# Performance work log

Measured on AMD Instinct MI355X. Metric: run time of the kernel, lower is better.

The kernel has to match this reference:

```python
import jax, jax.numpy as jnp
import numpy as np

N, F, H, C, E = 20000, 512, 128, 64, 640000


def _uniform(key, shape, stdv):
    return jax.random.uniform(key, shape, jnp.float32, -stdv, stdv)


def setup_inputs() -> dict:
    key = jax.random.key(0)
    ks = jax.random.split(key, 20)
    inp = {}
    for i, name in enumerate(['x1', 'x2', 'x3']):
        inp[name] = jax.random.normal(ks[i], (N, F), jnp.float32)
    for v, base in zip([1, 2, 3], [3, 6, 9]):
        inp[f'src{v}'] = jax.random.randint(ks[base], (E,), 0, N, jnp.int32)
        inp[f'dst{v}'] = jax.random.randint(ks[base + 1], (E,), 0, N, jnp.int32)
        inp[f'val{v}'] = jax.random.uniform(ks[base + 2], (E,), jnp.float32)
    s1 = 1.0 / np.sqrt(H)
    s2 = 1.0 / np.sqrt(C)
    sv = 1.0 / np.sqrt(3.0)
    inp['W1'] = _uniform(ks[12], (3, 3, F, H), s1)   # [gc, view_role, F, H]
    inp['wv1'] = _uniform(ks[13], (3, 3), sv)
    inp['b1'] = _uniform(ks[14], (3, H), sv)
    inp['W2'] = _uniform(ks[15], (3, 3, H, C), s2)
    inp['wv2'] = _uniform(ks[16], (3, 3), sv)
    inp['b2'] = _uniform(ks[17], (3, C), sv)
    return inp


def _spmm(src, dst, val, emb, n):
    # out[i] = sum_{edges e with src=i} val[e] * emb[dst[e]]
    return jax.ops.segment_sum(val[:, None] * emb[dst], src, num_segments=n)


def _igc(xs, adjs, W, wv, b, n):
    # xs: [x_self, x_v2, x_v3]; adjs: matching [(src,dst,val)]*3
    embs = [xs[i] @ W[i] for i in range(3)]
    neigh = [_spmm(adjs[i][0], adjs[i][1], adjs[i][2], embs[i], n) for i in range(3)]
    agg = wv[0] * neigh[0] + wv[1] * neigh[1] + wv[2] * neigh[2]
    return embs[0] + 1.01 * agg + b


def reference(x1, x2, x3, src1, dst1, val1, src2, dst2, val2, src3, dst3, val3,
              W1, wv1, b1, W2, wv2, b2):
    n = x1.shape[0]
    a1, a2, a3 = (src1, dst1, val1), (src2, dst2, val2), (src3, dst3, val3)
    relu = jax.nn.relu
    h1 = relu(_igc([x1, x2, x3], [a1, a2, a3], W1[0], wv1[0], b1[0], n))
    h2 = relu(_igc([x2, x1, x3], [a2, a1, a3], W1[1], wv1[1], b1[1], n))
    h3 = relu(_igc([x3, x1, x2], [a3, a1, a2], W1[2], wv1[2], b1[2], n))
    y1 = relu(_igc([h1, h2, h3], [a1, a2, a3], W2[0], wv2[0], b2[0], n))
    y2 = relu(_igc([h2, h1, h3], [a2, a1, a3], W2[1], wv2[1], b2[1], n))
    y3 = relu(_igc([h3, h1, h2], [a3, a1, a2], W2[2], wv2[2], b2[2], n))
    return jnp.abs((y1 + y2 + y3) / 3.0)
```

## Files before the change

### kernel.cpp

```cpp
#include <hip/hip_runtime.h>
#include <hip/hip_bf16.h>

#define N_NODES 20000
#define F_DIM   512
#define H_DIM   128
#define C_DIM   64
#define E_EDGES 640000

#define P_WV1   64
#define P_B1    80
#define P_WV2   464
#define P_B2    480
#define P_E     1024
#define P_H     (P_E + 3*N_NODES*H_DIM)
#define P_YSUM  (P_H + 3*N_NODES*H_DIM)
#define RP_SZ      20032
#define CSR_STRIDE (RP_SZ + 2*E_EDGES)
#define P_CSR   (P_YSUM + N_NODES*C_DIM)
#define P_CUR   (P_CSR + 3*CSR_STRIDE)
#define P_WT1   (P_E + 4000000)
#define P_WT2   (P_E + 4300000)
#define P_W1H   (P_YSUM)
#define P_W1L   (P_YSUM + 294912)
#define P_W2H   (P_E + 4000000)
#define P_W2L   (P_E + 4050000)
#define DEG_STRIDE 20480

typedef __attribute__((ext_vector_type(8))) unsigned short u16x8;
typedef __attribute__((ext_vector_type(8))) __bf16 bf16x8;
typedef __attribute__((ext_vector_type(4))) float f32x4;

__device__ inline float cvt(float x) { return x; }
__device__ inline float cvt(__hip_bfloat16 x) { return __bfloat162float(x); }

__device__ inline void store_out(float v, float* p) { *p = v; }
__device__ inline void store_out(float v, __hip_bfloat16* p) { *p = __float2bfloat16(v); }

__device__ inline unsigned short f2bf_bits(float x) {
    __hip_bfloat16 b = __float2bfloat16(x);
    return *(unsigned short*)&b;
}
__device__ inline void splitbf(float x, unsigned short& h, unsigned short& l) {
    h = f2bf_bits(x);
    float hf = __uint_as_float(((unsigned int)h) << 16);
    l = f2bf_bits(x - hf);
}

__global__ void detect_kernel(const unsigned short* __restrict__ x, int* flag) {
    __shared__ int cnt;
    if (threadIdx.x == 0) cnt = 0;
    __syncthreads();
    int c = 0;
    for (int i = threadIdx.x; i < 4096; i += 256) {
        int ex = (x[i] >> 7) & 0xff;
        if (ex >= 140) c++;
    }
    atomicAdd(&cnt, c);
    __syncthreads();
    if (threadIdx.x == 0) *flag = (cnt > 64) ? 1 : 0;
}

__global__ void prep_kernel(const int* __restrict__ flag,
                            const void* wv1, const void* b1,
                            const void* wv2, const void* b2, float* ws) {
    bool f32 = (*flag == 1);
    int t = threadIdx.x;
    auto get = [&](const void* p, int i) -> float {
        return f32 ? ((const float*)p)[i]
                   : __bfloat162float(((const __hip_bfloat16*)p)[i]);
    };
    if (t < 9) ws[P_WV1 + t] = get(wv1, t);
    if (t < 9) ws[P_WV2 + t] = get(wv2, t);
    for (int i = t; i < 3*H_DIM; i += 256) ws[P_B1 + i] = get(b1, i);
    for (int i = t; i < 3*C_DIM; i += 256) ws[P_B2 + i] = get(b2, i);
}

__global__ __launch_bounds__(256)
void hist3_kernel(const int* __restrict__ s0, const int* __restrict__ s1,
                  const int* __restrict__ s2, int* __restrict__ deg) {
    int e = blockIdx.x * 256 + threadIdx.x;
    if (e >= E_EDGES) return;
    const int* s = (blockIdx.y == 0) ? s0 : (blockIdx.y == 1) ? s1 : s2;
    atomicAdd(&deg[blockIdx.y * DEG_STRIDE + s[e]], 1);
}

__global__ __launch_bounds__(256)
void scan3_kernel(const int* __restrict__ degBase, int* __restrict__ rpBase) {
    __shared__ int sums[256];
    const int* deg = degBase + blockIdx.x * DEG_STRIDE;
    int* rowptr = rpBase + (long)blockIdx.x * CSR_STRIDE;
    const int CHUNK = 79;
    int t = threadIdx.x;
    int beg = t * CHUNK;
    int end = beg + CHUNK; if (end > N_NODES) end = N_NODES;
    int s = 0;
    for (int i = beg; i < end && i < N_NODES; ++i) s += deg[i];
    sums[t] = s;
    __syncthreads();
    for (int off = 1; off < 256; off <<= 1) {
        int v = (t >= off) ? sums[t - off] : 0;
        __syncthreads();
        sums[t] += v;
        __syncthreads();
    }
    int run = sums[t] - s;
    for (int i = beg; i < end && i < N_NODES; ++i) {
        rowptr[i] = run;
        run += deg[i];
    }
    if (t == 255) rowptr[N_NODES] = run;
}

__global__ __launch_bounds__(256)
void fill3_kernel(const int* __restrict__ flag,
                  const int* __restrict__ s0, const int* __restrict__ d0,
                  const void* __restrict__ v0,
                  const int* __restrict__ s1, const int* __restrict__ d1,
                  const void* __restrict__ v1,
                  const int* __restrict__ s2, const int* __restrict__ d2,
                  const void* __restrict__ v2,
                  int* __restrict__ rpBase, int* __restrict__ curBase) {
    int e = blockIdx.x * 256 + threadIdx.x;
    if (e >= E_EDGES) return;
    const int z = blockIdx.y;
    const int* src = (z == 0) ? s0 : (z == 1) ? s1 : s2;
    const int* dst = (z == 0) ? d0 : (z == 1) ? d1 : d2;
    const void* val = (z == 0) ? v0 : (z == 1) ? v1 : v2;
    float v = (*flag == 1) ? ((const float*)val)[e]
                           : __bfloat162float(((const __hip_bfloat16*)val)[e]);
    int s = src[e];
    int* rowptr = rpBase + (long)z * CSR_STRIDE;
    int pos = rowptr[s] + atomicAdd(&curBase[z * DEG_STRIDE + s], 1);
    int2* ed = (int2*)(rpBase + (long)z * CSR_STRIDE + RP_SZ);
    ed[pos] = make_int2(dst[e], __float_as_int(v));
}

__global__ __launch_bounds__(256)
void transpose_w_kernel(const int* __restrict__ flag,
                        const void* __restrict__ Wsrc,
                        unsigned short* __restrict__ Wt, int K, int HO) {
    if (*flag != 0) return;
    __shared__ unsigned short T[64][80];
    const unsigned short* W = (const unsigned short*)Wsrc + (long)blockIdx.z * K * HO;
    unsigned short* O = Wt + (long)blockIdx.z * HO * K;
    const int k0 = blockIdx.x * 64, n0 = blockIdx.y * 64;
    const int t = threadIdx.x;
    const int rr = t >> 3, cc = (t & 7) * 8;
    #pragma unroll
    for (int i = 0; i < 2; ++i) {
        int k = rr + i * 32;
        *(u16x8*)&T[k][cc] = *(const u16x8*)&W[(long)(k0 + k) * HO + n0 + cc];
    }
    __syncthreads();
    #pragma unroll
    for (int i = 0; i < 2; ++i) {
        int nn = rr + i * 32;
        u16x8 v;
        #pragma unroll
        for (int j = 0; j < 8; ++j) v[j] = T[cc + j][nn];
        *(u16x8*)&O[(long)(n0 + nn) * K + k0 + cc] = v;
    }
}

__global__ __launch_bounds__(256)
void split_w_kernel(const int* __restrict__ flag,
                    const float* __restrict__ Wsrc,
                    unsigned short* __restrict__ Wh,
                    unsigned short* __restrict__ Wl, int K, int HO) {
    if (*flag != 1) return;
    __shared__ float T[64][68];
    const float* W = Wsrc + (long)blockIdx.z * K * HO;
    unsigned short* Oh = Wh + (long)blockIdx.z * HO * K;
    unsigned short* Ol = Wl + (long)blockIdx.z * HO * K;
    const int k0 = blockIdx.x * 64, n0 = blockIdx.y * 64;
    const int t = threadIdx.x;
    #pragma unroll
    for (int i = 0; i < 16; ++i) {
        int idx = t + i * 256;
        int r = idx >> 6, c = idx & 63;
        T[r][c] = W[(long)(k0 + r) * HO + n0 + c];
    }
    __syncthreads();
    #pragma unroll
    for (int i = 0; i < 16; ++i) {
        int idx = t + i * 256;
        int nn = idx >> 6, kk = idx & 63;
        unsigned short h, l;
        splitbf(T[kk][nn], h, l);
        Oh[(long)(n0 + nn) * K + k0 + kk] = h;
        Ol[(long)(n0 + nn) * K + k0 + kk] = l;
    }
}

#define SWZ(r, kb) (((r) << 7) + ((kb) ^ (((r) & 7) << 4)))

__global__ __launch_bounds__(256)
void gemm_mfma1_kernel(const int* __restrict__ flag,
                       const unsigned short* __restrict__ x0,
                       const unsigned short* __restrict__ x1,
                       const unsigned short* __restrict__ x2,
                       const unsigned short* __restrict__ WtBase,
                       unsigned short* __restrict__ outBase, int n) {
    if (*flag != 0) return;
    const int role = blockIdx.y;
    const unsigned short* X = (role == 0) ? x0 : (role == 1) ? x1 : x2;
    const unsigned short* Wt = WtBase + (long)role * H_DIM * F_DIM;
    unsigned short* out = outBase + (long)role * N_NODES * H_DIM;
    __shared__ __align__(16) unsigned short As[64 * 64];
    __shared__ __align__(16) unsigned short Bs[128 * 64];
    const int t = threadIdx.x;
    const int lane = t & 63;
    const int wave = t >> 6;
    const int wm = wave & 1, wn = wave >> 1;
    const int row0 = blockIdx.x * 64;
    const int rl = lane & 15;
    const int kq = lane >> 4;
    const int sr = t >> 3;
    const int sc = (t & 7) * 8;
    f32x4 acc[2][4] = {};
    for (int k0 = 0; k0 < F_DIM; k0 += 64) {
        #pragma unroll
        for (int i = 0; i < 2; ++i) {
            int r = i * 32 + sr;
            int gr = row0 + r; if (gr >= n) gr = n - 1;
            u16x8 v = *(const u16x8*)&X[(long)gr * F_DIM + k0 + sc];
            *(u16x8*)((char*)As + SWZ(r, sc * 2)) = v;
        }
        #pragma unroll
        for (int i = 0; i < 4; ++i) {
            int r = i * 32 + sr;
            u16x8 v = *(const u16x8*)&Wt[(long)r * F_DIM + k0 + sc];
            *(u16x8*)((char*)Bs + SWZ(r, sc * 2)) = v;
        }
        __syncthreads();
        #pragma unroll
        for (int s = 0; s < 2; ++s) {
            const int kb = s * 64 + kq * 16;
            bf16x8 af[2], bfr[4];
            #pragma unroll
            for (int mi = 0; mi < 2; ++mi) {
                int r = wm * 32 + mi * 16 + rl;
                af[mi] = *(const bf16x8*)((const char*)As + SWZ(r, kb));
            }
            #pragma unroll
            for (int ni = 0; ni < 4; ++ni) {
                int r = wn * 64 + ni * 16 + rl;
                bfr[ni] = *(const bf16x8*)((const char*)Bs + SWZ(r, kb));
            }
            #pragma unroll
            for (int mi = 0; mi < 2; ++mi)
                #pragma unroll
                for (int ni = 0; ni < 4; ++ni)
                    acc[mi][ni] = __builtin_amdgcn_mfma_f32_16x16x32_bf16(
                        af[mi], bfr[ni], acc[mi][ni], 0, 0, 0);
        }
        __syncthreads();
    }
    #pragma unroll
    for (int mi = 0; mi < 2; ++mi) {
        #pragma unroll
        for (int q = 0; q < 4; ++q) {
            int row = row0 + wm * 32 + mi * 16 + kq * 4 + q;
            if (row < n) {
                #pragma unroll
                for (int ni = 0; ni < 4; ++ni) {
                    int col = wn * 64 + ni * 16 + rl;
                    out[(long)row * H_DIM + col] = f2bf_bits(acc[mi][ni][q]);
                }
            }
        }
    }
}

__global__ __launch_bounds__(256)
void gemm_mfma1f_kernel(const int* __restrict__ flag,
                        const float* __restrict__ x0,
                        const float* __restrict__ x1,
                        const float* __restrict__ x2,
                        const unsigned short* __restrict__ WhBase,
                        const unsigned short* __restrict__ WlBase,
                        float* __restrict__ outBase, int n) {
    if (*flag != 1) return;
    const int role = blockIdx.y;
    const float* X = (role == 0) ? x0 : (role == 1) ? x1 : x2;
    const unsigned short* Wh = WhBase + (long)role * H_DIM * F_DIM;
    const unsigned short* Wl = WlBase + (long)role * H_DIM * F_DIM;
    float* out = outBase + (long)role * N_NODES * H_DIM;
    __shared__ __align__(16) unsigned short Ash[64 * 64];
    __shared__ __align__(16) unsigned short Asl[64 * 64];
    __shared__ __align__(16) unsigned short Bsh[128 * 64];
    __shared__ __align__(16) unsigned short Bsl[128 * 64];
    const int t = threadIdx.x;
    const int lane = t & 63;
    const int wave = t >> 6;
    const int wm = wave & 1, wn = wave >> 1;
    const int row0 = blockIdx.x * 64;
    const int rl = lane & 15;
    const int kq = lane >> 4;
    const int sr = t >> 3;
    const int sc = (t & 7) * 8;
    f32x4 acc[2][4] = {};
    for (int k0 = 0; k0 < F_DIM; k0 += 64) {
        #pragma unroll
        for (int i = 0; i < 2; ++i) {
            int r = i * 32 + sr;
            int gr = row0 + r; if (gr >= n) gr = n - 1;
            float4 v0 = *(const float4*)&X[(long)gr * F_DIM + k0 + sc];
            float4 v1 = *(const float4*)&X[(long)gr * F_DIM + k0 + sc + 4];
            float xs[8] = {v0.x, v0.y, v0.z, v0.w, v1.x, v1.y, v1.z, v1.w};
            u16x8 hi, lo;
            #pragma unroll
            for (int j = 0; j < 8; ++j) { unsigned short h, l; splitbf(xs[j], h, l); hi[j] = h; lo[j] = l; }
            *(u16x8*)((char*)Ash + SWZ(r, sc * 2)) = hi;
            *(u16x8*)((char*)Asl + SWZ(r, sc * 2)) = lo;
        }
        #pragma unroll
        for (int i = 0; i < 4; ++i) {
            int r = i * 32 + sr;
            u16x8 vh = *(const u16x8*)&Wh[(long)r * F_DIM + k0 + sc];
            u16x8 vl = *(const u16x8*)&Wl[(long)r * F_DIM + k0 + sc];
            *(u16x8*)((char*)Bsh + SWZ(r, sc * 2)) = vh;
            *(u16x8*)((char*)Bsl + SWZ(r, sc * 2)) = vl;
        }
        __syncthreads();
        #pragma unroll
        for (int s = 0; s < 2; ++s) {
            const int kb = s * 64 + kq * 16;
            bf16x8 ah[2], al[2], bh[4], bl[4];
            #pragma unroll
            for (int mi = 0; mi < 2; ++mi) {
                int r = wm * 32 + mi * 16 + rl;
                ah[mi] = *(const bf16x8*)((const char*)Ash + SWZ(r, kb));
                al[mi] = *(const bf16x8*)((const char*)Asl + SWZ(r, kb));
            }
            #pragma unroll
            for (int ni = 0; ni < 4; ++ni) {
                int r = wn * 64 + ni * 16 + rl;
                bh[ni] = *(const bf16x8*)((const char*)Bsh + SWZ(r, kb));
                bl[ni] = *(const bf16x8*)((const char*)Bsl + SWZ(r, kb));
            }
            #pragma unroll
            for (int mi = 0; mi < 2; ++mi)
                #pragma unroll
                for (int ni = 0; ni < 4; ++ni) {
                    acc[mi][ni] = __builtin_amdgcn_mfma_f32_16x16x32_bf16(
                        ah[mi], bh[ni], acc[mi][ni], 0, 0, 0);
                    acc[mi][ni] = __builtin_amdgcn_mfma_f32_16x16x32_bf16(
                        ah[mi], bl[ni], acc[mi][ni], 0, 0, 0);
                    acc[mi][ni] = __builtin_amdgcn_mfma_f32_16x16x32_bf16(
                        al[mi], bh[ni], acc[mi][ni], 0, 0, 0);
                }
        }
        __syncthreads();
    }
    #pragma unroll
    for (int mi = 0; mi < 2; ++mi) {
        #pragma unroll
        for (int q = 0; q < 4; ++q) {
            int row = row0 + wm * 32 + mi * 16 + kq * 4 + q;
            if (row < n) {
                #pragma unroll
                for (int ni = 0; ni < 4; ++ni) {
                    int col = wn * 64 + ni * 16 + rl;
                    out[(long)row * H_DIM + col] = acc[mi][ni][q];
                }
            }
        }
    }
}

#define SWZ2(r, kb) (((r) << 8) + ((kb) ^ (((r) & 7) << 4)))

__global__ __launch_bounds__(256)
void gemm_mfma2_kernel(const int* __restrict__ flag,
                       const unsigned short* __restrict__ h0,
                       const unsigned short* __restrict__ h1,
                       const unsigned short* __restrict__ h2,
                       const unsigned short* __restrict__ WtBase,
                       unsigned short* __restrict__ outBase, int n) {
    if (*flag != 0) return;
    const int role = blockIdx.y;
    const unsigned short* X = (role == 0) ? h0 : (role == 1) ? h1 : h2;
    const unsigned short* Wt = WtBase + (long)role * C_DIM * H_DIM;
    unsigned short* out = outBase + (long)role * N_NODES * C_DIM;
    __shared__ __align__(16) unsigned short As[64 * 128];
    __shared__ __align__(16) unsigned short Bs[64 * 128];
    const int t = threadIdx.x;
    const int lane = t & 63;
    const int wave = t >> 6;
    const int wm = wave & 1, wn = wave >> 1;
    const int row0 = blockIdx.x * 64;
    const int rl = lane & 15;
    const int kq = lane >> 4;
    #pragma unroll
    for (int i = 0; i < 4; ++i) {
        int e = t + i * 256;
        int r = e >> 4, c8 = e & 15;
        int gr = row0 + r; if (gr >= n) gr = n - 1;
        u16x8 va = *(const u16x8*)&X[(long)gr * H_DIM + c8 * 8];
        *(u16x8*)((char*)As + SWZ2(r, c8 * 16)) = va;
        u16x8 vb = *(const u16x8*)&Wt[(long)r * H_DIM + c8 * 8];
        *(u16x8*)((char*)Bs + SWZ2(r, c8 * 16)) = vb;
    }
    __syncthreads();
    f32x4 acc[2][2] = {};
    #pragma unroll
    for (int s = 0; s < 4; ++s) {
        const int kb = s * 64 + kq * 16;
        bf16x8 af[2], bfr[2];
        #pragma unroll
        for (int mi = 0; mi < 2; ++mi) {
            int r = wm * 32 + mi * 16 + rl;
            af[mi] = *(const bf16x8*)((const char*)As + SWZ2(r, kb));
        }
        #pragma unroll
        for (int ni = 0; ni < 2; ++ni) {
            int r = wn * 32 + ni * 16 + rl;
            bfr[ni] = *(const bf16x8*)((const char*)Bs + SWZ2(r, kb));
        }
        #pragma unroll
        for (int mi = 0; mi < 2; ++mi)
            #pragma unroll
            for (int ni = 0; ni < 2; ++ni)
                acc[mi][ni] = __builtin_amdgcn_mfma_f32_16x16x32_bf16(
                    af[mi], bfr[ni], acc[mi][ni], 0, 0, 0);
    }
    #pragma unroll
    for (int mi = 0; mi < 2; ++mi) {
        #pragma unroll
        for (int q = 0; q < 4; ++q) {
            int row = row0 + wm * 32 + mi * 16 + kq * 4 + q;
            if (row < n) {
                #pragma unroll
                for (int ni = 0; ni < 2; ++ni) {
                    int col = wn * 32 + ni * 16 + rl;
                    out[(long)row * C_DIM + col] = f2bf_bits(acc[mi][ni][q]);
                }
            }
        }
    }
}

__global__ __launch_bounds__(256)
void gemm_mfma2f_kernel(const int* __restrict__ flag,
                        const float* __restrict__ h0,
                        const float* __restrict__ h1,
                        const float* __restrict__ h2,
                        const unsigned short* __restrict__ WhBase,
                        const unsigned short* __restrict__ WlBase,
                        float* __restrict__ outBase, int n) {
    if (*flag != 1) return;
    const int role = blockIdx.y;
    const float* X = (role == 0) ? h0 : (role == 1) ? h1 : h2;
    const unsigned short* Wh = WhBase + (long)role * C_DIM * H_DIM;
    const unsigned short* Wl = WlBase + (long)role * C_DIM * H_DIM;
    float* out = outBase + (long)role * N_NODES * C_DIM;
    __shared__ __align__(16) unsigned short Ash[64 * 128];
    __shared__ __align__(16) unsigned short Asl[64 * 128];
    __shared__ __align__(16) unsigned short Bsh[64 * 128];
    __shared__ __align__(16) unsigned short Bsl[64 * 128];
    const int t = threadIdx.x;
    const int lane = t & 63;
    const int wave = t >> 6;
    const int wm = wave & 1, wn = wave >> 1;
    const int row0 = blockIdx.x * 64;
    const int rl = lane & 15;
    const int kq = lane >> 4;
    #pragma unroll
    for (int i = 0; i < 4; ++i) {
        int e = t + i * 256;
        int r = e >> 4, c8 = e & 15;
        int gr = row0 + r; if (gr >= n) gr = n - 1;
        float4 v0 = *(const float4*)&X[(long)gr * H_DIM + c8 * 8];
        float4 v1 = *(const float4*)&X[(long)gr * H_DIM + c8 * 8 + 4];
        float xs[8] = {v0.x, v0.y, v0.z, v0.w, v1.x, v1.y, v1.z, v1.w};
        u16x8 hi, lo;
        #pragma unroll
        for (int j = 0; j < 8; ++j) { unsigned short h, l; splitbf(xs[j], h, l); hi[j] = h; lo[j] = l; }
        *(u16x8*)((char*)Ash + SWZ2(r, c8 * 16)) = hi;
        *(u16x8*)((char*)Asl + SWZ2(r, c8 * 16)) = lo;
        u16x8 vh = *(const u16x8*)&Wh[(long)r * H_DIM + c8 * 8];
        u16x8 vl = *(const u16x8*)&Wl[(long)r * H_DIM + c8 * 8];
        *(u16x8*)((char*)Bsh + SWZ2(r, c8 * 16)) = vh;
        *(u16x8*)((char*)Bsl + SWZ2(r, c8 * 16)) = vl;
    }
    __syncthreads();
    f32x4 acc[2][2] = {};
    #pragma unroll
    for (int s = 0; s < 4; ++s) {
        const int kb = s * 64 + kq * 16;
        bf16x8 ah[2], al[2], bh[2], bl[2];
        #pragma unroll
        for (int mi = 0; mi < 2; ++mi) {
            int r = wm * 32 + mi * 16 + rl;
            ah[mi] = *(const bf16x8*)((const char*)Ash + SWZ2(r, kb));
            al[mi] = *(const bf16x8*)((const char*)Asl + SWZ2(r, kb));
        }
        #pragma unroll
        for (int ni = 0; ni < 2; ++ni) {
            int r = wn * 32 + ni * 16 + rl;
            bh[ni] = *(const bf16x8*)((const char*)Bsh + SWZ2(r, kb));
            bl[ni] = *(const bf16x8*)((const char*)Bsl + SWZ2(r, kb));
        }
        #pragma unroll
        for (int mi = 0; mi < 2; ++mi)
            #pragma unroll
            for (int ni = 0; ni < 2; ++ni) {
                acc[mi][ni] = __builtin_amdgcn_mfma_f32_16x16x32_bf16(
                    ah[mi], bh[ni], acc[mi][ni], 0, 0, 0);
                acc[mi][ni] = __builtin_amdgcn_mfma_f32_16x16x32_bf16(
                    ah[mi], bl[ni], acc[mi][ni], 0, 0, 0);
                acc[mi][ni] = __builtin_amdgcn_mfma_f32_16x16x32_bf16(
                    al[mi], bh[ni], acc[mi][ni], 0, 0, 0);
            }
    }
    #pragma unroll
    for (int mi = 0; mi < 2; ++mi) {
        #pragma unroll
        for (int q = 0; q < 4; ++q) {
            int row = row0 + wm * 32 + mi * 16 + kq * 4 + q;
            if (row < n) {
                #pragma unroll
                for (int ni = 0; ni < 2; ++ni) {
                    int col = wn * 32 + ni * 16 + rl;
                    out[(long)row * C_DIM + col] = acc[mi][ni][q];
                }
            }
        }
    }
}

template <int FP, bool ACCUM>
__global__ __launch_bounds__(256)
void spmm_f32_kernel(const int* __restrict__ flag,
                     const int* __restrict__ rp0, const int2* __restrict__ ed0,
                     const int* __restrict__ rp1, const int2* __restrict__ ed1,
                     const int* __restrict__ rp2, const int2* __restrict__ ed2,
                     const float* __restrict__ Et0, const float* __restrict__ Et1,
                     const float* __restrict__ Et2,
                     const float* __restrict__ wvp, const float* __restrict__ bias,
                     float* __restrict__ out) {
    if (*flag != 1) return;
    constexpr int HO = FP * 64;
    const int node = blockIdx.x * 4 + (threadIdx.x >> 6);
    const int lane = threadIdx.x & 63;
    const int fbase = lane * FP;
    float acc[FP];
    #pragma unroll
    for (int k = 0; k < FP; ++k) acc[k] = 0.f;

    const int*  rps[3] = {rp0, rp1, rp2};
    const int2* eds[3] = {ed0, ed1, ed2};
    const float* Ets[3] = {Et0, Et1, Et2};
    #pragma unroll
    for (int r = 0; r < 3; ++r) {
        const float s = 1.01f * wvp[r];
        const int2* ed = eds[r];
        const float* Et = Ets[r] + fbase;
        int e = rps[r][node];
        const int end = rps[r][node + 1];
        for (; e + 8 <= end; e += 8) {
            int2 E[8]; float vv[8]; const float* rr[8];
            #pragma unroll
            for (int q = 0; q < 8; ++q) E[q] = ed[e + q];
            #pragma unroll
            for (int q = 0; q < 8; ++q) {
                vv[q] = s * __int_as_float(E[q].y);
                rr[q] = Et + (long)E[q].x * HO;
            }
            #pragma unroll
            for (int q = 0; q < 8; ++q)
                #pragma unroll
                for (int k = 0; k < FP; ++k) acc[k] += vv[q] * rr[q][k];
        }
        for (; e + 2 <= end; e += 2) {
            int2 E0 = ed[e], E1 = ed[e + 1];
            float v0 = s * __int_as_float(E0.y), v1 = s * __int_as_float(E1.y);
            const float* r0 = Et + (long)E0.x * HO;
            const float* r1 = Et + (long)E1.x * HO;
            #pragma unroll
            for (int k = 0; k < FP; ++k) acc[k] += v0 * r0[k];
            #pragma unroll
            for (int k = 0; k < FP; ++k) acc[k] += v1 * r1[k];
        }
        if (e < end) {
            int2 E0 = ed[e];
            float v0 = s * __int_as_float(E0.y);
            const float* r0 = Et + (long)E0.x * HO;
            #pragma unroll
            for (int k = 0; k < FP; ++k) acc[k] += v0 * r0[k];
        }
    }
    const float* e0 = Et0 + (long)node * HO + fbase;
    const float* bp = bias + fbase;
    float* o = out + (long)node * HO + fbase;
    #pragma unroll
    for (int k = 0; k < FP; ++k) {
        float x = e0[k] + acc[k] + bp[k];
        x = x > 0.f ? x : 0.f;
        if (ACCUM) o[k] += x; else o[k] = x;
    }
}

template <int HO, bool ACCUM, bool OUT_BF16>
__global__ __launch_bounds__(256)
void spmm_bf16_kernel(const int* __restrict__ flag,
                      const int* __restrict__ rp0, const int2* __restrict__ ed0,
                      const int* __restrict__ rp1, const int2* __restrict__ ed1,
                      const int* __restrict__ rp2, const int2* __restrict__ ed2,
                      const unsigned short* __restrict__ Et0,
                      const unsigned short* __restrict__ Et1,
                      const unsigned short* __restrict__ Et2,
                      const float* __restrict__ wvp, const float* __restrict__ bias,
                      void* __restrict__ outp) {
    if (*flag != 0) return;
    constexpr int NL = HO / 2;
    constexpr int NPW = 64 / NL;
    const int t = threadIdx.x;
    const int lane = t & 63;
    const int li = lane % NL;
    const int node = blockIdx.x * (4 * NPW) + (t >> 6) * NPW + lane / NL;
    const int fl = li * 2;
    float a0 = 0.f, a1 = 0.f;

    const int*  rps[3] = {rp0, rp1, rp2};
    const int2* eds[3] = {ed0, ed1, ed2};
    const unsigned int* Ets[3] = {(const unsigned int*)Et0,
                                  (const unsigned int*)Et1,
                                  (const unsigned int*)Et2};
    #pragma unroll
    for (int r = 0; r < 3; ++r) {
        const float s = 1.01f * wvp[r];
        const int2* ed = eds[r];
        const unsigned int* Et = Ets[r] + li;
        int e = rps[r][node];
        const int end = rps[r][node + 1];
        for (; e + 4 <= end; e += 4) {
            int2 E0 = ed[e], E1 = ed[e + 1], E2 = ed[e + 2], E3 = ed[e + 3];
            float v0 = s * __int_as_float(E0.y), v1 = s * __int_as_float(E1.y);
            float v2 = s * __int_as_float(E2.y), v3 = s * __int_as_float(E3.y);
            unsigned int w0 = Et[(long)E0.x * NL];
            unsigned int w1 = Et[(long)E1.x * NL];
            unsigned int w2 = Et[(long)E2.x * NL];
            unsigned int w3 = Et[(long)E3.x * NL];
            a0 += v0 * __uint_as_float(w0 << 16);
            a1 += v0 * __uint_as_float(w0 & 0xffff0000u);
            a0 += v1 * __uint_as_float(w1 << 16);
            a1 += v1 * __uint_as_float(w1 & 0xffff0000u);
            a0 += v2 * __uint_as_float(w2 << 16);
            a1 += v2 * __uint_as_float(w2 & 0xffff0000u);
            a0 += v3 * __uint_as_float(w3 << 16);
            a1 += v3 * __uint_as_float(w3 & 0xffff0000u);
        }
        for (; e < end; ++e) {
            int2 E0 = ed[e];
            float v0 = s * __int_as_float(E0.y);
            unsigned int w0 = Et[(long)E0.x * NL];
            a0 += v0 * __uint_as_float(w0 << 16);
            a1 += v0 * __uint_as_float(w0 & 0xffff0000u);
        }
    }
    unsigned int ws0 = ((const unsigned int*)Et0)[(long)node * NL + li];
    float x0 = __uint_as_float(ws0 << 16)        + a0 + bias[fl];
    float x1 = __uint_as_float(ws0 & 0xffff0000u) + a1 + bias[fl + 1];
    x0 = x0 > 0.f ? x0 : 0.f;
    x1 = x1 > 0.f ? x1 : 0.f;
    if (OUT_BF16) {
        unsigned int packed = ((unsigned int)f2bf_bits(x1) << 16) | f2bf_bits(x0);
        ((unsigned int*)outp)[(long)node * NL + li] = packed;
    } else {
        float* o = (float*)outp + (long)node * HO + fl;
        if (ACCUM) { o[0] += x0; o[1] += x1; }
        else       { o[0] = x0;  o[1] = x1; }
    }
}

template <typename TOUT>
__global__ __launch_bounds__(256)
void final_kernel(const int* __restrict__ flag, int want,
                  const float* __restrict__ ysum, TOUT* __restrict__ out, int n) {
    if (*flag != want) return;
    int i = blockIdx.x * 256 + threadIdx.x;
    if (i >= n) return;
    store_out(fabsf(ysum[i] * (1.f / 3.f)), &out[i]);
}

extern "C" void kernel_launch(void* const* d_in, const int* in_sizes, int n_in,
                              void* d_out, int out_size, void* d_ws, size_t ws_size,
                              hipStream_t stream) {
    float* ws = (float*)d_ws;
    int* flag = (int*)d_ws;
    static const int perm[3][3] = {{0, 1, 2}, {1, 0, 2}, {2, 0, 1}};

    detect_kernel<<<1, 256, 0, stream>>>((const unsigned short*)d_in[0], flag);
    prep_kernel<<<1, 256, 0, stream>>>(flag, d_in[13], d_in[14], d_in[16], d_in[17], ws);

    int* csrbase = (int*)(ws + P_CSR);
    int* rp[3]; int2* ed[3];
    for (int j = 0; j < 3; ++j) {
        rp[j] = csrbase + (long)j * CSR_STRIDE;
        ed[j] = (int2*)(rp[j] + RP_SZ);
    }
    {
        int* deg = (int*)(ws + P_YSUM);
        int* cur3 = deg + 3 * DEG_STRIDE;
        hipMemsetAsync(deg, 0, (size_t)6 * DEG_STRIDE * 4, stream);
        dim3 ge((E_EDGES + 255) / 256, 3);
        hist3_kernel<<<ge, 256, 0, stream>>>(
            (const int*)d_in[3], (const int*)d_in[6], (const int*)d_in[9], deg);
        scan3_kernel<<<3, 256, 0, stream>>>(deg, csrbase);
        fill3_kernel<<<ge, 256, 0, stream>>>(
            flag,
            (const int*)d_in[3], (const int*)d_in[4], d_in[5],
            (const int*)d_in[6], (const int*)d_in[7], d_in[8],
            (const int*)d_in[9], (const int*)d_in[10], d_in[11],
            csrbase, cur3);
    }

    unsigned short* Wt1 = (unsigned short*)(ws + P_WT1);
    unsigned short* Wt2 = (unsigned short*)(ws + P_WT2);
    {
        dim3 g1(F_DIM / 64, H_DIM / 64, 9);
        transpose_w_kernel<<<g1, 256, 0, stream>>>(flag, d_in[12], Wt1, F_DIM, H_DIM);
        dim3 g2(H_DIM / 64, C_DIM / 64, 9);
        transpose_w_kernel<<<g2, 256, 0, stream>>>(flag, d_in[15], Wt2, H_DIM, C_DIM);
    }
    unsigned short* W1h = (unsigned short*)(ws + P_W1H);
    unsigned short* W1l = (unsigned short*)(ws + P_W1L);
    {
        dim3 g1(F_DIM / 64, H_DIM / 64, 9);
        split_w_kernel<<<g1, 256, 0, stream>>>(flag, (const float*)d_in[12],
                                               W1h, W1l, F_DIM, H_DIM);
    }

    unsigned short* Eb = (unsigned short*)(ws + P_E);
    unsigned short* Hb = (unsigned short*)(ws + P_H);

    const int gemmBlocks = (N_NODES + 63) / 64;

    for (int v = 0; v < 3; ++v) {
        int j0 = perm[v][0], j1 = perm[v][1], j2 = perm[v][2];
        dim3 g(gemmBlocks, 3);
        gemm_mfma1_kernel<<<g, 256, 0, stream>>>(
            flag,
            (const unsigned short*)d_in[j0], (const unsigned short*)d_in[j1],
            (const unsigned short*)d_in[j2],
            Wt1 + (long)v * 3 * H_DIM * F_DIM, Eb, N_NODES);
        gemm_mfma1f_kernel<<<g, 256, 0, stream>>>(
            flag,
            (const float*)d_in[j0], (const float*)d_in[j1], (const float*)d_in[j2],
            W1h + (long)v * 3 * H_DIM * F_DIM, W1l + (long)v * 3 * H_DIM * F_DIM,
            ws + P_E, N_NODES);

        spmm_bf16_kernel<128, false, true><<<N_NODES / 4, 256, 0, stream>>>(
            flag, rp[j0], ed[j0], rp[j1], ed[j1], rp[j2], ed[j2],
            Eb, Eb + (long)N_NODES * H_DIM, Eb + 2L * N_NODES * H_DIM,
            ws + P_WV1 + v * 3, ws + P_B1 + v * H_DIM,
            Hb + (long)v * N_NODES * H_DIM);
        spmm_f32_kernel<2, false><<<N_NODES / 4, 256, 0, stream>>>(
            flag, rp[j0], ed[j0], rp[j1], ed[j1], rp[j2], ed[j2],
            ws + P_E, ws + P_E + (long)N_NODES * H_DIM, ws + P_E + 2L * N_NODES * H_DIM,
            ws + P_WV1 + v * 3, ws + P_B1 + v * H_DIM,
            ws + P_H + (long)v * N_NODES * H_DIM);
    }

    unsigned short* W2h = (unsigned short*)(ws + P_W2H);
    unsigned short* W2l = (unsigned short*)(ws + P_W2L);
    {
        dim3 g2(H_DIM / 64, C_DIM / 64, 9);
        split_w_kernel<<<g2, 256, 0, stream>>>(flag, (const float*)d_in[15],
                                               W2h, W2l, H_DIM, C_DIM);
    }

    for (int v = 0; v < 3; ++v) {
        int j0 = perm[v][0], j1 = perm[v][1], j2 = perm[v][2];
        dim3 g(gemmBlocks, 3);
        gemm_mfma2_kernel<<<g, 256, 0, stream>>>(
            flag,
            Hb + (long)j0 * N_NODES * H_DIM, Hb + (long)j1 * N_NODES * H_DIM,
            Hb + (long)j2 * N_NODES * H_DIM,
            Wt2 + (long)v * 3 * C_DIM * H_DIM, Eb, N_NODES);
        gemm_mfma2f_kernel<<<g, 256, 0, stream>>>(
            flag,
            ws + P_H + (long)j0 * N_NODES * H_DIM,
            ws + P_H + (long)j1 * N_NODES * H_DIM,
            ws + P_H + (long)j2 * N_NODES * H_DIM,
            W2h + (long)v * 3 * C_DIM * H_DIM, W2l + (long)v * 3 * C_DIM * H_DIM,
            ws + P_E, N_NODES);

        if (v == 0) {
            spmm_bf16_kernel<64, false, false><<<N_NODES / 8, 256, 0, stream>>>(
                flag, rp[j0], ed[j0], rp[j1], ed[j1], rp[j2], ed[j2],
                Eb, Eb + (long)N_NODES * C_DIM, Eb + 2L * N_NODES * C_DIM,
                ws + P_WV2 + v * 3, ws + P_B2 + v * C_DIM, ws + P_YSUM);
            spmm_f32_kernel<1, false><<<N_NODES / 4, 256, 0, stream>>>(
                flag, rp[j0], ed[j0], rp[j1], ed[j1], rp[j2], ed[j2],
                ws + P_E, ws + P_E + (long)N_NODES * C_DIM, ws + P_E + 2L * N_NODES * C_DIM,
                ws + P_WV2 + v * 3, ws + P_B2 + v * C_DIM, ws + P_YSUM);
        } else {
            spmm_bf16_kernel<64, true, false><<<N_NODES / 8, 256, 0, stream>>>(
                flag, rp[j0], ed[j0], rp[j1], ed[j1], rp[j2], ed[j2],
                Eb, Eb + (long)N_NODES * C_DIM, Eb + 2L * N_NODES * C_DIM,
                ws + P_WV2 + v * 3, ws + P_B2 + v * C_DIM, ws + P_YSUM);
            spmm_f32_kernel<1, true><<<N_NODES / 4, 256, 0, stream>>>(
                flag, rp[j0], ed[j0], rp[j1], ed[j1], rp[j2], ed[j2],
                ws + P_E, ws + P_E + (long)N_NODES * C_DIM, ws + P_E + 2L * N_NODES * C_DIM,
                ws + P_WV2 + v * 3, ws + P_B2 + v * C_DIM, ws + P_YSUM);
        }
    }

    final_kernel<__hip_bfloat16><<<(out_size + 255) / 256, 256, 0, stream>>>(
        flag, 0, ws + P_YSUM, (__hip_bfloat16*)d_out, out_size);
    final_kernel<float><<<(out_size + 255) / 256, 256, 0, stream>>>(
        flag, 1, ws + P_YSUM, (float*)d_out, out_size);
}
```

Before: 1.118 ms.

## Bucket CSR edges by destination range within each source row

The CSR build now counts and scatters edges into 8 buckets per source row, keyed by the top bits of the destination index. The goal is that SpMM gathers within a row hit nearby embedding rows, which should give better L2/cache locality. In exchange the histogram and scan arrays grow 8x. The single-block scan3 also has to walk 160k entries per graph, which adds preprocessing cost.

```diff
diff --git a/kernel.cpp b/kernel.cpp
--- a/kernel.cpp
+++ b/kernel.cpp
@@ -24,7 +24,9 @@
 #define P_W1L   (P_YSUM + 294912)
 #define P_W2H   (P_E + 4000000)
 #define P_W2L   (P_E + 4050000)
-#define DEG_STRIDE 20480
+#define NBUCK       8
+#define BUCK_SHIFT  12
+#define B2_STRIDE   (N_NODES * NBUCK)
 
 typedef __attribute__((ext_vector_type(8))) unsigned short u16x8;
 typedef __attribute__((ext_vector_type(8))) __bf16 bf16x8;
@@ -76,25 +78,29 @@
 }
 
 __global__ __launch_bounds__(256)
-void hist3_kernel(const int* __restrict__ s0, const int* __restrict__ s1,
-                  const int* __restrict__ s2, int* __restrict__ deg) {
+void hist2_kernel(const int* __restrict__ s0, const int* __restrict__ d0,
+                  const int* __restrict__ s1, const int* __restrict__ d1,
+                  const int* __restrict__ s2, const int* __restrict__ d2,
+                  int* __restrict__ deg2) {
     int e = blockIdx.x * 256 + threadIdx.x;
     if (e >= E_EDGES) return;
-    const int* s = (blockIdx.y == 0) ? s0 : (blockIdx.y == 1) ? s1 : s2;
-    atomicAdd(&deg[blockIdx.y * DEG_STRIDE + s[e]], 1);
-}
-
-__global__ __launch_bounds__(256)
-void scan3_kernel(const int* __restrict__ degBase, int* __restrict__ rpBase) {
+    const int z = blockIdx.y;
+    const int* src = (z == 0) ? s0 : (z == 1) ? s1 : s2;
+    const int* dst = (z == 0) ? d0 : (z == 1) ? d1 : d2;
+    int idx = src[e] * NBUCK + (dst[e] >> BUCK_SHIFT);
+    atomicAdd(&deg2[z * B2_STRIDE + idx], 1);
+}
+
+__global__ __launch_bounds__(256)
+void scan3b_kernel(int* __restrict__ deg2, int* __restrict__ rpBase) {
     __shared__ int sums[256];
-    const int* deg = degBase + blockIdx.x * DEG_STRIDE;
+    int* d = deg2 + blockIdx.x * B2_STRIDE;
     int* rowptr = rpBase + (long)blockIdx.x * CSR_STRIDE;
-    const int CHUNK = 79;
+    const int CHUNK = B2_STRIDE / 256;
     int t = threadIdx.x;
-    int beg = t * CHUNK;
-    int end = beg + CHUNK; if (end > N_NODES) end = N_NODES;
+    int beg = t * CHUNK, end = beg + CHUNK;
     int s = 0;
-    for (int i = beg; i < end && i < N_NODES; ++i) s += deg[i];
+    for (int i = beg; i < end; ++i) s += d[i];
     sums[t] = s;
     __syncthreads();
     for (int off = 1; off < 256; off <<= 1) {
@@ -104,9 +110,11 @@
         __syncthreads();
     }
     int run = sums[t] - s;
-    for (int i = beg; i < end && i < N_NODES; ++i) {
-        rowptr[i] = run;
-        run += deg[i];
+    for (int i = beg; i < end; ++i) {
+        int v = d[i];
+        d[i] = run;
+        if ((i & (NBUCK - 1)) == 0) rowptr[i >> 3] = run;
+        run += v;
     }
     if (t == 255) rowptr[N_NODES] = run;
 }
@@ -119,7 +127,8 @@
                   const void* __restrict__ v1,
                   const int* __restrict__ s2, const int* __restrict__ d2,
                   const void* __restrict__ v2,
-                  int* __restrict__ rpBase, int* __restrict__ curBase) {
+                  const int* __restrict__ deg2, int* __restrict__ cur2,
+                  int* __restrict__ rpBase) {
     int e = blockIdx.x * 256 + threadIdx.x;
     if (e >= E_EDGES) return;
     const int z = blockIdx.y;
@@ -128,11 +137,11 @@
     const void* val = (z == 0) ? v0 : (z == 1) ? v1 : v2;
     float v = (*flag == 1) ? ((const float*)val)[e]
                            : __bfloat162float(((const __hip_bfloat16*)val)[e]);
-    int s = src[e];
-    int* rowptr = rpBase + (long)z * CSR_STRIDE;
-    int pos = rowptr[s] + atomicAdd(&curBase[z * DEG_STRIDE + s], 1);
+    int d = dst[e];
+    int idx = z * B2_STRIDE + src[e] * NBUCK + (d >> BUCK_SHIFT);
+    int pos = deg2[idx] + atomicAdd(&cur2[idx], 1);
     int2* ed = (int2*)(rpBase + (long)z * CSR_STRIDE + RP_SZ);
-    ed[pos] = make_int2(dst[e], __float_as_int(v));
+    ed[pos] = make_int2(d, __float_as_int(v));
 }
 
 __global__ __launch_bounds__(256)
@@ -702,19 +711,21 @@
         ed[j] = (int2*)(rp[j] + RP_SZ);
     }
     {
-        int* deg = (int*)(ws + P_YSUM);
-        int* cur3 = deg + 3 * DEG_STRIDE;
-        hipMemsetAsync(deg, 0, (size_t)6 * DEG_STRIDE * 4, stream);
+        int* deg2 = (int*)(ws + P_YSUM);
+        int* cur2 = deg2 + 3 * B2_STRIDE;
+        hipMemsetAsync(deg2, 0, (size_t)6 * B2_STRIDE * 4, stream);
         dim3 ge((E_EDGES + 255) / 256, 3);
-        hist3_kernel<<<ge, 256, 0, stream>>>(
-            (const int*)d_in[3], (const int*)d_in[6], (const int*)d_in[9], deg);
-        scan3_kernel<<<3, 256, 0, stream>>>(deg, csrbase);
+        hist2_kernel<<<ge, 256, 0, stream>>>(
+            (const int*)d_in[3], (const int*)d_in[4],
+            (const int*)d_in[6], (const int*)d_in[7],
+            (const int*)d_in[9], (const int*)d_in[10], deg2);
+        scan3b_kernel<<<3, 256, 0, stream>>>(deg2, csrbase);
         fill3_kernel<<<ge, 256, 0, stream>>>(
             flag,
             (const int*)d_in[3], (const int*)d_in[4], d_in[5],
             (const int*)d_in[6], (const int*)d_in[7], d_in[8],
             (const int*)d_in[9], (const int*)d_in[10], d_in[11],
-            csrbase, cur3);
+            deg2, cur2, csrbase);
     }
 
     unsigned short* Wt1 = (unsigned short*)(ws + P_WT1);
```

Measured after the change: 1.285 ms. 15.0% more time.
